# Performance work log

Measured on AMD Instinct MI355X. Metric: run time of the kernel, lower is better.

Reference implementation:

```python
import jax, jax.numpy as jnp
import numpy as np

ABITS = 4
WBITS = 4
BN_EPS = 1e-5


def _ste(x, q):
    # straight-through estimator: forward q, backward identity
    return x + jax.lax.stop_gradient(q - x)


def act_quant(x):
    # unsigned activation quantization to ABITS (clipped-ReLU style, as in NIPQ quantized act)
    levels = (1 << ABITS) - 1  # 15
    xc = jnp.clip(x, 0.0, 1.0)
    q = jnp.round(xc * levels) / levels
    return _ste(xc, q)


def weight_quant(w):
    # symmetric per-tensor weight quantization to WBITS
    n = (1 << (WBITS - 1)) - 1  # 7
    alpha = jnp.max(jnp.abs(w)) + 1e-12
    wc = jnp.clip(w / alpha, -1.0, 1.0)
    q = jnp.round(wc * n) / n * alpha
    return _ste(w, q)


def conv3x3(x, w):
    # NCHW, OIHW, stride 1, padding 1
    return jax.lax.conv_general_dilated(
        x, w, window_strides=(1, 1), padding=((1, 1), (1, 1)),
        dimension_numbers=('NCHW', 'OIHW', 'NCHW'))


def batchnorm(x, gamma, beta):
    # training-mode BN: batch statistics over (N,H,W)
    mean = jnp.mean(x, axis=(0, 2, 3), keepdims=True)
    var = jnp.var(x, axis=(0, 2, 3), keepdims=True)
    xhat = (x - mean) * jax.lax.rsqrt(var + BN_EPS)
    return xhat * gamma[None, :, None, None] + beta[None, :, None, None]


def setup_inputs() -> dict:
    key = jax.random.key(0)
    k = jax.random.split(key, 3)
    C = 128
    x = jax.random.normal(k[0], (64, C, 56, 56), dtype=jnp.float32)
    w1 = jax.random.normal(k[1], (C, C, 3, 3), dtype=jnp.float32) * 0.05
    w2 = jax.random.normal(k[2], (C, C, 3, 3), dtype=jnp.float32) * 0.05
    return {
        'x': x, 'w1': w1, 'w2': w2,
        'gamma1': jnp.ones((C,), jnp.float32), 'beta1': jnp.zeros((C,), jnp.float32),
        'gamma2': jnp.ones((C,), jnp.float32), 'beta2': jnp.zeros((C,), jnp.float32),
    }


def reference(x, w1, w2, gamma1, beta1, gamma2, beta2):
    identity = x
    out = act_quant(x)
    out = conv3x3(out, weight_quant(w1))
    out = batchnorm(out, gamma1, beta1)
    out = act_quant(out)
    out = conv3x3(out, weight_quant(w2))
    out = batchnorm(out, gamma2, beta2)
    return out + identity
```

## Files before the change

### kernel.cpp

```cpp
#include <hip/hip_runtime.h>

#define CH    128
#define IMG   56
#define PADW  58
#define HWSZ  3136
#define NPIX  200704
#define WELEMS 147456
#define BNEPS 1e-5f
#define PADB  430592
#define YOFF  27557888u
#define Y2OFF_B 51380224u
#define WQ1OFF_B 78938112u
#define IMGB  802816u

#define BPIX   224
#define NBLK   (NPIX / BPIX)
#define STRIPB 44544
#define STRIPC 2784
#define BBASE  44544
#define REDOFF 77312
#define SMEMSZ 78336

typedef float f32x4 __attribute__((ext_vector_type(4)));
typedef int   i32x4 __attribute__((ext_vector_type(4)));
typedef short short8 __attribute__((ext_vector_type(8)));
typedef _Float16 f16;

__device__ __forceinline__ void async16(const void* g, void* l) {
  __builtin_amdgcn_global_load_lds(
      (const __attribute__((address_space(1))) unsigned int*)g,
      (__attribute__((address_space(3))) unsigned int*)l, 16, 0, 0);
}
__device__ __forceinline__ void bn_inline(int lin, const float* stats, const unsigned* abits,
                                          const float* g, const float* b, float* bnpS) {
  if (lin < 128) {
    const float inv = 1.f / (float)NPIX;
    float gs   = (__uint_as_float(*abits) + 1e-12f) * (1.f / 105.f);
    float mean = stats[lin] * inv;
    float var  = fmaxf(stats[CH + lin] * inv - mean * mean, 0.f);
    float sc   = g[lin] * gs * rsqrtf(gs * gs * var + BNEPS);
    bnpS[lin]      = sc;
    bnpS[CH + lin] = b[lin] - sc * mean;
  }
}
__device__ __forceinline__ void halo_zero(unsigned char* qb, int lin) {
  for (int i = lin; i < 1824; i += 256) {
    size_t off;
    if (i < 464)      off = (size_t)i * 16;
    else if (i < 928) off = (size_t)57 * PADW * 128 + (size_t)(i - 464) * 16;
    else {
      int j = i - 928, loc = j >> 3, sub = j & 7;
      int row = 1 + (loc >> 1), col = (loc & 1) ? 57 : 0;
      off = ((size_t)row * PADW + col) * 128 + (size_t)sub * 16;
    }
    *(uint4*)(qb + off) = (uint4){0u, 0u, 0u, 0u};
  }
}

__global__ void k_wmax(const float* __restrict__ w1, const float* __restrict__ w2,
                       unsigned* __restrict__ alpha_bits) {
  int idx = blockIdx.x * 256 + threadIdx.x;
  float m1 = 0.f, m2 = 0.f;
  for (int i = idx; i < WELEMS; i += gridDim.x * 256) {
    m1 = fmaxf(m1, fabsf(w1[i]));
    m2 = fmaxf(m2, fabsf(w2[i]));
  }
#pragma unroll
  for (int off = 32; off > 0; off >>= 1) {
    m1 = fmaxf(m1, __shfl_xor(m1, off));
    m2 = fmaxf(m2, __shfl_xor(m2, off));
  }
  __shared__ float s1[4], s2[4];
  int wave = threadIdx.x >> 6;
  if ((threadIdx.x & 63) == 0) { s1[wave] = m1; s2[wave] = m2; }
  __syncthreads();
  if (threadIdx.x == 0) {
    m1 = fmaxf(fmaxf(s1[0], s1[1]), fmaxf(s1[2], s1[3]));
    m2 = fmaxf(fmaxf(s2[0], s2[1]), fmaxf(s2[2], s2[3]));
    atomicMax(&alpha_bits[0], __float_as_uint(m1));
    atomicMax(&alpha_bits[1], __float_as_uint(m2));
  }
}

__global__ void k_wquant(const float* __restrict__ w1, const float* __restrict__ w2,
                         const unsigned* __restrict__ alpha_bits,
                         unsigned char* __restrict__ wq1, unsigned char* __restrict__ wq2) {
  int idx = blockIdx.x * 256 + threadIdx.x;
  int t = idx >= WELEMS;
  int j = t ? idx - WELEMS : idx;
  int kk  = j >> 14;
  int rem = j & 16383;
  int co = rem >> 7, ci = rem & 127;
  float alpha = __uint_as_float(alpha_bits[t]) + 1e-12f;
  float v  = (t ? w2 : w1)[co * 1152 + ci * 9 + kk];
  float wc = fminf(fmaxf(v / alpha, -1.f), 1.f);
  int q = (int)rintf(wc * 7.f);
  (t ? wq2 : wq1)[j] = (unsigned char)(q & 0xFF);
}

__global__ void k_actq(const float* __restrict__ x, unsigned char* __restrict__ qx) {
  __shared__ float tile[128][33];
  int n = blockIdx.z, p0 = blockIdx.x * 32;
  int tx = threadIdx.x, ty = threadIdx.y, lin = ty * 32 + tx;
  unsigned char* qb = qx + (size_t)n * PADB;
  if (blockIdx.x == 0) halo_zero(qb, lin);
  const float* xs = x + (size_t)n * CH * HWSZ;
#pragma unroll
  for (int r = 0; r < 16; ++r) {
    int c = ty + r * 8;
    float v = xs[(size_t)c * HWSZ + p0 + tx];
    v = fminf(fmaxf(v, 0.f), 1.f);
    tile[c][tx] = rintf(v * 15.f);
  }
  __syncthreads();
  int p = lin >> 3, q8 = lin & 7;
  int pl = p0 + p;
  int h = pl / IMG, w = pl - h * IMG;
  unsigned u[4];
#pragma unroll
  for (int k = 0; k < 4; ++k) {
    unsigned b0 = (unsigned)(int)tile[q8 * 16 + k * 4 + 0][p];
    unsigned b1 = (unsigned)(int)tile[q8 * 16 + k * 4 + 1][p];
    unsigned b2 = (unsigned)(int)tile[q8 * 16 + k * 4 + 2][p];
    unsigned b3 = (unsigned)(int)tile[q8 * 16 + k * 4 + 3][p];
    u[k] = b0 | (b1 << 8) | (b2 << 16) | (b3 << 24);
  }
  *(uint4*)(qb + ((size_t)(h + 1) * PADW + (w + 1)) * 128 + q8 * 16) =
      (uint4){u[0], u[1], u[2], u[3]};
}

#define CONV_SETUP2                                                              \
  const int tid  = threadIdx.x;                                                  \
  const int lane = tid & 63;                                                     \
  const int quad = lane >> 4, lrow = lane & 15;                                  \
  const int m_base = ((tid >> 6) >> 1) * 112, n_base = ((tid >> 6) & 1) * 64;    \
  int sbase[7];                                                                  \
  _Pragma("unroll")                                                              \
  for (int mi = 0; mi < 7; ++mi) {                                               \
    int row = m_base + mi * 16 + lrow;                                           \
    sbase[mi] = (row / 56) * 58 + (row % 56);                                    \
  }                                                                              \
  int boff[4], bldsoff[4];                                                       \
  _Pragma("unroll")                                                              \
  for (int i = 0; i < 4; ++i) {                                                  \
    int c = i * 256 + tid;                                                       \
    int r = c >> 3;                                                              \
    boff[i] = r * 128 + ((c & 7) ^ (r & 7)) * 16;                                \
    bldsoff[i] = (i * 256 + (tid & ~63)) * 16;                                   \
  }                                                                              \
  i32x4 acc[7][4];                                                               \
  _Pragma("unroll")                                                              \
  for (int mi = 0; mi < 7; ++mi)                                                 \
    _Pragma("unroll")                                                            \
    for (int ni = 0; ni < 4; ++ni) acc[mi][ni] = (i32x4){0, 0, 0, 0};

#define CONV_STAGE_PRO(STRIPSRC, WQ)                                             \
  _Pragma("unroll")                                                              \
  for (int it = 0; it < 11; ++it) {                                              \
    int u = it * 256 + tid;                                                      \
    if (u < STRIPC) {                                                            \
      int s = u >> 3, cc = u & 7;                                                \
      async16((STRIPSRC) + s * 128 + ((cc ^ (s & 7)) << 4),                      \
              smem + (it * 256 + (tid & ~63)) * 16);                             \
    }                                                                            \
  }                                                                              \
  _Pragma("unroll")                                                              \
  for (int i = 0; i < 4; ++i) async16((WQ) + boff[i], smem + BBASE + bldsoff[i]);\
  __syncthreads();

#define CONV_KLOOP2(WQ)                                                          \
  _Pragma("unroll")                                                              \
  for (int kk = 0; kk < 9; ++kk) {                                               \
    if (kk < 8) {                                 \
      const int kn = kk + 1;                                                     \
      char* nb = smem + BBASE + ((kn & 1) << 14);                                \
      _Pragma("unroll")                                                          \
      for (int i = 0; i < 4; ++i)                                                \
        async16((WQ) + kn * 16384 + boff[i], nb + bldsoff[i]);                   \
    }                                                                            \
    const char* Bs = smem + BBASE + ((kk & 1) << 14);                            \
    const int dkk = (kk / 3) * 58 + (kk % 3);                                    \
    int aaddr[7];                                                                \
    _Pragma("unroll")                                                            \
    for (int mi = 0; mi < 7; ++mi) {                                             \
      int s = sbase[mi] + dkk;                                                   \
      aaddr[mi] = (s << 7) + ((quad << 4) ^ ((s & 7) << 4));                     \
    }                                                                            \
    __builtin_amdgcn_s_setprio(1);                                               \
    _Pragma("unroll")                                                            \
    for (int j = 0; j < 2; ++j) {                                                \
      i32x4 af[7], bf[4];                                                        \
      _Pragma("unroll")                                                          \
      for (int mi = 0; mi < 7; ++mi)                                             \
        af[mi] = *(const i32x4*)(smem + (aaddr[mi] ^ (j << 6)));                 \
      _Pragma("unroll")                                                          \
      for (int ni = 0; ni < 4; ++ni) {                                           \
        int brow = n_base + ni * 16 + lrow;                                      \
        bf[ni] = *(const i32x4*)(Bs + brow * 128 +                               \
                                 (((j << 6) | (quad << 4)) ^ ((brow & 7) << 4)));\
      }                                                                          \
      _Pragma("unroll")                                                          \
      for (int mi = 0; mi < 7; ++mi)                                             \
        _Pragma("unroll")                                                        \
        for (int ni = 0; ni < 4; ++ni)                                           \
          acc[mi][ni] = __builtin_amdgcn_mfma_i32_16x16x64_i8(af[mi], bf[ni], acc[mi][ni], 0, 0, 0); \
    }                                                                            \
    __builtin_amdgcn_s_setprio(0);                                               \
    __syncthreads();                                                             \
  }

__global__ __launch_bounds__(256, 2)
void k_conv(const unsigned char* __restrict__ act, const unsigned char* __restrict__ wq,
            short* __restrict__ ylo, short* __restrict__ yhi, int nsplit,
            float* __restrict__ stats) {
  __shared__ __align__(16) char smem[SMEMSZ];
  const int bidx = ((blockIdx.x & 7) * 112) + (blockIdx.x >> 3);
  const int n = bidx / 14, br = bidx % 14;
  const unsigned char* strip = act + (size_t)n * PADB + (size_t)br * 4 * PADW * 128;
  CONV_SETUP2
  CONV_STAGE_PRO(strip, wq)
  CONV_KLOOP2(wq)
  short* yb = (n < nsplit ? ylo + (size_t)n * HWSZ * CH
                          : yhi + (size_t)(n - nsplit) * HWSZ * CH);
  const int pbase = br * BPIX;
  float lsum[4] = {0.f, 0.f, 0.f, 0.f}, lsq[4] = {0.f, 0.f, 0.f, 0.f};
#pragma unroll
  for (int mi = 0; mi < 7; ++mi) {
    int prow = pbase + m_base + mi * 16 + quad * 4;
#pragma unroll
    for (int ni = 0; ni < 4; ++ni) {
      int co = n_base + ni * 16 + lrow;
#pragma unroll
      for (int rg = 0; rg < 4; ++rg) {
        float v = (float)acc[mi][ni][rg];
        yb[(size_t)(prow + rg) * CH + co] = (short)fminf(fmaxf(v, -32767.f), 32767.f);
        lsum[ni] += v; lsq[ni] += v * v;
      }
    }
  }
#pragma unroll
  for (int ni = 0; ni < 4; ++ni) {
    lsum[ni] += __shfl_xor(lsum[ni], 16); lsum[ni] += __shfl_xor(lsum[ni], 32);
    lsq[ni]  += __shfl_xor(lsq[ni], 16);  lsq[ni]  += __shfl_xor(lsq[ni], 32);
  }
  __syncthreads();
  float* red = (float*)(smem + REDOFF);
  red[tid] = 0.f;
  __syncthreads();
  if (quad == 0) {
#pragma unroll
    for (int ni = 0; ni < 4; ++ni) {
      int co = n_base + ni * 16 + lrow;
      atomicAdd(&red[co], lsum[ni]);
      atomicAdd(&red[CH + co], lsq[ni]);
    }
  }
  __syncthreads();
  atomicAdd(&stats[tid], red[tid]);
}

__global__ void k_bnq(const short* __restrict__ y, const float* __restrict__ stats,
                      const unsigned* __restrict__ abits, const float* __restrict__ g,
                      const float* __restrict__ b, unsigned char* __restrict__ q) {
  __shared__ float bnpS[256];
  int tid = threadIdx.x;
  bn_inline(tid, stats, abits, g, b, bnpS);
  if (blockIdx.x < 64) halo_zero(q + (size_t)blockIdx.x * PADB, tid);
  __syncthreads();
  size_t i = (size_t)blockIdx.x * 256 + tid;
  short8 v0 = ((const short8*)y)[i * 2];
  short8 v1 = ((const short8*)y)[i * 2 + 1];
  int c0 = (int)((i * 16) & (CH - 1));
  int pix = (int)(i >> 3);
  int n = pix / HWSZ, l = pix - n * HWSZ;
  int h = l / IMG, w = l - h * IMG;
  unsigned u[4] = {0u, 0u, 0u, 0u};
#pragma unroll
  for (int j = 0; j < 8; ++j) {
    float a0 = (float)v0[j] * bnpS[c0 + j] + bnpS[CH + c0 + j];
    float a1 = (float)v1[j] * bnpS[c0 + 8 + j] + bnpS[CH + c0 + 8 + j];
    unsigned q0 = (unsigned)(int)rintf(fminf(fmaxf(a0, 0.f), 1.f) * 15.f);
    unsigned q1 = (unsigned)(int)rintf(fminf(fmaxf(a1, 0.f), 1.f) * 15.f);
    u[j >> 2]       |= q0 << (8 * (j & 3));
    u[2 + (j >> 2)] |= q1 << (8 * (j & 3));
  }
  *(uint4*)(q + (size_t)n * PADB + ((h + 1) * PADW + (w + 1)) * 128 + c0) =
      (uint4){u[0], u[1], u[2], u[3]};
}

__global__ void k_fin(const short* __restrict__ ylo, const short* __restrict__ yhi, int nsplit,
                      const float* __restrict__ stats,
                      const unsigned* __restrict__ abits, const float* __restrict__ g,
                      const float* __restrict__ b, const float* __restrict__ x,
                      float* __restrict__ out, int img0) {
  __shared__ float bnpS[256];
  __shared__ float tile[128][33];
  int tx = threadIdx.x, ty = threadIdx.y, lin = ty * 32 + tx;
  bn_inline(lin, stats, abits, g, b, bnpS);
  __syncthreads();
  int n = img0 + blockIdx.z, p0 = blockIdx.x * 32;
  int p = lin >> 3, c0 = (lin & 7) * 16;
  const short* ybase = (n < nsplit ? ylo + (size_t)n * HWSZ * CH
                                   : yhi + (size_t)(n - nsplit) * HWSZ * CH);
  const short* ys = ybase + (size_t)(p0 + p) * CH + c0;
  short8 v0 = *(const short8*)ys;
  short8 v1 = *(const short8*)(ys + 8);
#pragma unroll
  for (int j = 0; j < 8; ++j) {
    tile[c0 + j][p]     = (float)v0[j] * bnpS[c0 + j]     + bnpS[CH + c0 + j];
    tile[c0 + 8 + j][p] = (float)v1[j] * bnpS[c0 + 8 + j] + bnpS[CH + c0 + 8 + j];
  }
  __syncthreads();
  const float* xs = x + (size_t)n * CH * HWSZ;
  float*       os = out + (size_t)n * CH * HWSZ;
#pragma unroll
  for (int r = 0; r < 16; ++r) {
    int c = ty + r * 8;
    size_t a = (size_t)c * HWSZ + p0 + tx;
    os[a] = tile[c][tx] + xs[a];
  }
}

__global__ __launch_bounds__(256, 2)
void k_conv_out63(const unsigned char* __restrict__ act, const unsigned char* __restrict__ wq,
                  const float* __restrict__ stats, const unsigned* __restrict__ abits,
                  const float* __restrict__ g, const float* __restrict__ b,
                  const float* __restrict__ x, float* __restrict__ out) {
  __shared__ __align__(16) char smem[SMEMSZ];
  __shared__ float bnpS[256];
  bn_inline(threadIdx.x, stats, abits, g, b, bnpS);
  const int br = blockIdx.x;
  const unsigned char* strip = act + (size_t)br * 4 * PADW * 128;
  CONV_SETUP2
  CONV_STAGE_PRO(strip, wq)
  CONV_KLOOP2(wq)
  __syncthreads();
  f16 (*tile)[228] = (f16(*)[228])smem;
#pragma unroll
  for (int ni = 0; ni < 4; ++ni) {
    int co = n_base + ni * 16 + lrow;
    float sc = bnpS[co], sh = bnpS[CH + co];
#pragma unroll
    for (int mi = 0; mi < 7; ++mi) {
      int pr = m_base + mi * 16 + quad * 4;
#pragma unroll
      for (int rg = 0; rg < 4; ++rg)
        tile[co][pr + rg] = (f16)((float)acc[mi][ni][rg] * sc + sh);
    }
  }
  __syncthreads();
  int c = tid >> 1, seg = tid & 1;
  int pl0 = br * BPIX + seg * 112;
  size_t gb = ((size_t)63 * CH + c) * HWSZ + pl0;
  const float* xp = x + gb;
  float* op = out + gb;
  const f16* tr = &tile[c][seg * 112];
#pragma unroll
  for (int j = 0; j < 112; j += 4) {
    f32x4 xv = *(const f32x4*)(xp + j);
    f32x4 ov;
    ov[0] = (float)tr[j]     + xv[0];
    ov[1] = (float)tr[j + 1] + xv[1];
    ov[2] = (float)tr[j + 2] + xv[2];
    ov[3] = (float)tr[j + 3] + xv[3];
    *(f32x4*)(op + j) = ov;
  }
}

extern "C" void kernel_launch(void* const* d_in, const int* in_sizes, int n_in,
                              void* d_out, int out_size, void* d_ws, size_t ws_size,
                              hipStream_t stream) {
  (void)in_sizes; (void)n_in; (void)out_size;
  const float* x  = (const float*)d_in[0];
  const float* w1 = (const float*)d_in[1];
  const float* w2 = (const float*)d_in[2];
  const float* g1 = (const float*)d_in[3];
  const float* b1 = (const float*)d_in[4];
  const float* g2 = (const float*)d_in[5];
  const float* b2 = (const float*)d_in[6];
  float* out = (float*)d_out;

  char* dob = (char*)d_out;
  unsigned char* q1p = (unsigned char*)dob;
  unsigned char* q2p = (unsigned char*)dob;
  short* y1 = (short*)(dob + YOFF);

  char* ws = (char*)d_ws;
  unsigned* alpha_bits = (unsigned*)ws;
  float* stats1 = (float*)(ws + 256);
  float* stats2 = (float*)(ws + 1280);

  hipMemsetAsync(ws, 0, 4608, stream);
  k_wmax  <<<64, 256, 0, stream>>>(w1, w2, alpha_bits);

  if (ws_size >= 51679744u) {
    unsigned char* wq1 = (unsigned char*)(ws + 4608);
    unsigned char* wq2 = (unsigned char*)(ws + 152064);
    short* y2 = (short*)(ws + 299520);
    k_wquant<<<2 * WELEMS / 256, 256, 0, stream>>>(w1, w2, alpha_bits, wq1, wq2);
    k_actq  <<<dim3(98, 1, 64), dim3(32, 8), 0, stream>>>(x, q1p);
    k_conv  <<<NBLK, 256, 0, stream>>>(q1p, wq1, y1, y1, 64, stats1);
    k_bnq   <<<NPIX * CH / 4096, 256, 0, stream>>>(y1, stats1, alpha_bits + 0, g1, b1, q2p);
    k_conv  <<<NBLK, 256, 0, stream>>>(q2p, wq2, y2, y2, 64, stats2);
    k_fin   <<<dim3(98, 1, 64), dim3(32, 8), 0, stream>>>(y2, y2, 64, stats2, alpha_bits + 1, g2, b2, x, out, 0);
    return;
  }

  unsigned char* wq1 = (unsigned char*)(dob + WQ1OFF_B);
  unsigned char* wq2 = (unsigned char*)(ws + 4608);
  short* y2lo = (short*)(dob + Y2OFF_B);
  k_wquant<<<2 * WELEMS / 256, 256, 0, stream>>>(w1, w2, alpha_bits, wq1, wq2);
  k_actq  <<<dim3(98, 1, 64), dim3(32, 8), 0, stream>>>(x, q1p);
  k_conv  <<<NBLK, 256, 0, stream>>>(q1p, wq1, y1, y1, 64, stats1);
  k_bnq   <<<NPIX * CH / 4096, 256, 0, stream>>>(y1, stats1, alpha_bits + 0, g1, b1, q2p);

  if (ws_size >= 152064u + 32u * IMGB) {
    short* y2hi = (short*)(ws + 152064);
    k_conv <<<NBLK, 256, 0, stream>>>(q2p, wq2, y2lo, y2hi, 32, stats2);
    k_fin <<<dim3(98, 1, 32), dim3(32, 8), 0, stream>>>(y2lo, y2hi, 32, stats2, alpha_bits + 1, g2, b2, x, out, 0);
    k_fin <<<dim3(98, 1, 32), dim3(32, 8), 0, stream>>>(y2lo, y2hi, 32, stats2, alpha_bits + 1, g2, b2, x, out, 32);
  } else if (ws_size >= 152064u + 16u * IMGB) {
    short* y2hi = (short*)(ws + 152064);
    k_conv <<<NBLK, 256, 0, stream>>>(q2p, wq2, y2lo, y2hi, 48, stats2);
    k_fin <<<dim3(98, 1, 32), dim3(32, 8), 0, stream>>>(y2lo, y2hi, 48, stats2, alpha_bits + 1, g2, b2, x, out, 0);
    k_fin <<<dim3(98, 1, 16), dim3(32, 8), 0, stream>>>(y2lo, y2hi, 48, stats2, alpha_bits + 1, g2, b2, x, out, 32);
    k_fin <<<dim3(98, 1, 16), dim3(32, 8), 0, stream>>>(y2lo, y2hi, 48, stats2, alpha_bits + 1, g2, b2, x, out, 48);
  } else {
    unsigned char* q63p = (unsigned char*)(ws + 152064);
    k_conv <<<NBLK, 256, 0, stream>>>(q2p, wq2, y2lo, y2lo, 64, stats2);
    hipMemcpyAsync(q63p, q2p + (size_t)63 * PADB, PADB, hipMemcpyDeviceToDevice, stream);
    k_fin <<<dim3(98, 1, 32), dim3(32, 8), 0, stream>>>(y2lo, y2lo, 64, stats2, alpha_bits + 1, g2, b2, x, out, 0);
    k_fin <<<dim3(98, 1, 16), dim3(32, 8), 0, stream>>>(y2lo, y2lo, 64, stats2, alpha_bits + 1, g2, b2, x, out, 32);
    k_fin <<<dim3(98, 1,  8), dim3(32, 8), 0, stream>>>(y2lo, y2lo, 64, stats2, alpha_bits + 1, g2, b2, x, out, 48);
    k_fin <<<dim3(98, 1,  4), dim3(32, 8), 0, stream>>>(y2lo, y2lo, 64, stats2, alpha_bits + 1, g2, b2, x, out, 56);
    k_fin <<<dim3(98, 1,  2), dim3(32, 8), 0, stream>>>(y2lo, y2lo, 64, stats2, alpha_bits + 1, g2, b2, x, out, 60);
    k_fin <<<dim3(98, 1,  1), dim3(32, 8), 0, stream>>>(y2lo, y2lo, 64, stats2, alpha_bits + 1, g2, b2, x, out, 62);
    k_conv_out63<<<14, 256, 0, stream>>>(q63p, wq2, stats2, alpha_bits + 1, g2, b2, x, out);
  }
}
```

Before: 324.5 us.

## Load conv weight fragments directly from global memory, dropping LDS B staging

```diff
diff --git a/kernel.cpp b/kernel.cpp
--- a/kernel.cpp
+++ b/kernel.cpp
@@ -17,9 +17,9 @@
 #define NBLK   (NPIX / BPIX)
 #define STRIPB 44544
 #define STRIPC 2784
-#define BBASE  44544
-#define REDOFF 77312
-#define SMEMSZ 78336
+#define REDOFF 44544
+#define SMEMC  45568
+#define SMEM63 58368
 
 typedef float f32x4 __attribute__((ext_vector_type(4)));
 typedef int   i32x4 __attribute__((ext_vector_type(4)));
@@ -140,21 +140,17 @@
     int row = m_base + mi * 16 + lrow;                                           \
     sbase[mi] = (row / 56) * 58 + (row % 56);                                    \
   }                                                                              \
-  int boff[4], bldsoff[4];                                                       \
+  int bgoff[4];                                                                  \
   _Pragma("unroll")                                                              \
-  for (int i = 0; i < 4; ++i) {                                                  \
-    int c = i * 256 + tid;                                                       \
-    int r = c >> 3;                                                              \
-    boff[i] = r * 128 + ((c & 7) ^ (r & 7)) * 16;                                \
-    bldsoff[i] = (i * 256 + (tid & ~63)) * 16;                                   \
-  }                                                                              \
+  for (int ni = 0; ni < 4; ++ni)                                                 \
+    bgoff[ni] = (n_base + ni * 16 + lrow) * 128 + (quad << 4);                   \
   i32x4 acc[7][4];                                                               \
   _Pragma("unroll")                                                              \
   for (int mi = 0; mi < 7; ++mi)                                                 \
     _Pragma("unroll")                                                            \
     for (int ni = 0; ni < 4; ++ni) acc[mi][ni] = (i32x4){0, 0, 0, 0};
 
-#define CONV_STAGE_PRO(STRIPSRC, WQ)                                             \
+#define CONV_STAGE_PRO(STRIPSRC)                                                 \
   _Pragma("unroll")                                                              \
   for (int it = 0; it < 11; ++it) {                                              \
     int u = it * 256 + tid;                                                      \
@@ -164,21 +160,11 @@
               smem + (it * 256 + (tid & ~63)) * 16);                             \
     }                                                                            \
   }                                                                              \
-  _Pragma("unroll")                                                              \
-  for (int i = 0; i < 4; ++i) async16((WQ) + boff[i], smem + BBASE + bldsoff[i]);\
-  __syncthreads();
-
-#define CONV_KLOOP2(WQ)                                                          \
+  __syncthreads();
+
+#define CONV_KLOOP3(WQ)                                                          \
   _Pragma("unroll")                                                              \
   for (int kk = 0; kk < 9; ++kk) {                                               \
-    if (kk < 8) {                                 \
-      const int kn = kk + 1;                                                     \
-      char* nb = smem + BBASE + ((kn & 1) << 14);                                \
-      _Pragma("unroll")                                                          \
-      for (int i = 0; i < 4; ++i)                                                \
-        async16((WQ) + kn * 16384 + boff[i], nb + bldsoff[i]);                   \
-    }                                                                            \
-    const char* Bs = smem + BBASE + ((kk & 1) << 14);                            \
     const int dkk = (kk / 3) * 58 + (kk % 3);                                    \
     int aaddr[7];                                                                \
     _Pragma("unroll")                                                            \
@@ -186,40 +172,36 @@
       int s = sbase[mi] + dkk;                                                   \
       aaddr[mi] = (s << 7) + ((quad << 4) ^ ((s & 7) << 4));                     \
     }                                                                            \
-    __builtin_amdgcn_s_setprio(1);                                               \
     _Pragma("unroll")                                                            \
     for (int j = 0; j < 2; ++j) {                                                \
-      i32x4 af[7], bf[4];                                                        \
+      i32x4 bf[4], af[7];                                                        \
+      _Pragma("unroll")                                                          \
+      for (int ni = 0; ni < 4; ++ni)                                             \
+        bf[ni] = *(const i32x4*)((WQ) + kk * 16384 + bgoff[ni] + (j << 6));      \
       _Pragma("unroll")                                                          \
       for (int mi = 0; mi < 7; ++mi)                                             \
         af[mi] = *(const i32x4*)(smem + (aaddr[mi] ^ (j << 6)));                 \
-      _Pragma("unroll")                                                          \
-      for (int ni = 0; ni < 4; ++ni) {                                           \
-        int brow = n_base + ni * 16 + lrow;                                      \
-        bf[ni] = *(const i32x4*)(Bs + brow * 128 +                               \
-                                 (((j << 6) | (quad << 4)) ^ ((brow & 7) << 4)));\
-      }                                                                          \
+      __builtin_amdgcn_s_setprio(1);                                             \
       _Pragma("unroll")                                                          \
       for (int mi = 0; mi < 7; ++mi)                                             \
         _Pragma("unroll")                                                        \
         for (int ni = 0; ni < 4; ++ni)                                           \
           acc[mi][ni] = __builtin_amdgcn_mfma_i32_16x16x64_i8(af[mi], bf[ni], acc[mi][ni], 0, 0, 0); \
+      __builtin_amdgcn_s_setprio(0);                                             \
     }                                                                            \
-    __builtin_amdgcn_s_setprio(0);                                               \
-    __syncthreads();                                                             \
   }
 
 __global__ __launch_bounds__(256, 2)
 void k_conv(const unsigned char* __restrict__ act, const unsigned char* __restrict__ wq,
             short* __restrict__ ylo, short* __restrict__ yhi, int nsplit,
             float* __restrict__ stats) {
-  __shared__ __align__(16) char smem[SMEMSZ];
+  __shared__ __align__(16) char smem[SMEMC];
   const int bidx = ((blockIdx.x & 7) * 112) + (blockIdx.x >> 3);
   const int n = bidx / 14, br = bidx % 14;
   const unsigned char* strip = act + (size_t)n * PADB + (size_t)br * 4 * PADW * 128;
   CONV_SETUP2
-  CONV_STAGE_PRO(strip, wq)
-  CONV_KLOOP2(wq)
+  CONV_STAGE_PRO(strip)
+  CONV_KLOOP3(wq)
   short* yb = (n < nsplit ? ylo + (size_t)n * HWSZ * CH
                           : yhi + (size_t)(n - nsplit) * HWSZ * CH);
   const int pbase = br * BPIX;
@@ -326,14 +308,14 @@
                   const float* __restrict__ stats, const unsigned* __restrict__ abits,
                   const float* __restrict__ g, const float* __restrict__ b,
                   const float* __restrict__ x, float* __restrict__ out) {
-  __shared__ __align__(16) char smem[SMEMSZ];
+  __shared__ __align__(16) char smem[SMEM63];
   __shared__ float bnpS[256];
   bn_inline(threadIdx.x, stats, abits, g, b, bnpS);
   const int br = blockIdx.x;
   const unsigned char* strip = act + (size_t)br * 4 * PADW * 128;
   CONV_SETUP2
-  CONV_STAGE_PRO(strip, wq)
-  CONV_KLOOP2(wq)
+  CONV_STAGE_PRO(strip)
+  CONV_KLOOP3(wq)
   __syncthreads();
   f16 (*tile)[228] = (f16(*)[228])smem;
 #pragma unroll
```

After: 356.6 us. 9.9% more time.
